# Performance work log

Hardware: AMD Instinct MI355X
Metric: run time of the kernel (lower is better)

The kernel has to match this reference:

```python
import jax, jax.numpy as jnp
from jax import lax
import numpy as np

CONF_THRES = 0.25
IOU_THRES = 0.45
MAX_OUT = 100  # max_output_boxes_per_class
N_BOXES = 25200  # YOLO 640x640 anchor count


def setup_inputs() -> dict:
    key = jax.random.key(0)
    kb, ks = jax.random.split(key)
    u = jax.random.uniform(kb, (N_BOXES, 4), dtype=jnp.float32)
    # build realistic corner boxes (x1,y1,x2,y2) on a 640x640 canvas
    cx, cy = u[:, 0] * 640.0, u[:, 1] * 640.0
    w = u[:, 2] * 60.0 + 4.0
    h = u[:, 3] * 60.0 + 4.0
    boxes = jnp.stack([cx - w / 2, cy - h / 2, cx + w / 2, cy + h / 2], axis=1)
    scores = jax.random.uniform(ks, (N_BOXES,), dtype=jnp.float32)
    return {"boxes": boxes, "scores": scores}


def _nms_indices(boxes, scores):
    """Greedy NMS. Returns (indices[MAX_OUT] into original boxes, valid[MAX_OUT] mask).
    Confidence filtering (scores > conf_thres) is done by masking to -inf so shapes stay static."""
    n = scores.shape[0]
    s = jnp.where(scores > CONF_THRES, scores, -jnp.inf)
    order = jnp.argsort(-s)               # descending score order
    b = boxes[order]                      # [N,4] sorted boxes
    s = s[order]                          # [N] sorted scores
    area = jnp.maximum(b[:, 2] - b[:, 0], 0.0) * jnp.maximum(b[:, 3] - b[:, 1], 0.0)
    pos = jnp.arange(n)

    def body(i, suppressed):
        keep_i = (~suppressed[i]) & jnp.isfinite(s[i])
        lt = jnp.maximum(b[i, :2], b[:, :2])   # intersection top-left
        rb = jnp.minimum(b[i, 2:], b[:, 2:])   # intersection bottom-right
        wh = jnp.maximum(rb - lt, 0.0)
        inter = wh[:, 0] * wh[:, 1]
        iou = inter / (area[i] + area - inter + 1e-9)
        return suppressed | (keep_i & (pos > i) & (iou > IOU_THRES))

    suppressed = lax.fori_loop(0, n, body, jnp.zeros((n,), bool))
    keep = (~suppressed) & jnp.isfinite(s)
    # pack first MAX_OUT kept (already in score order) into fixed-size output
    rank = jnp.cumsum(keep) - 1
    slot = jnp.where(keep & (rank < MAX_OUT), rank, MAX_OUT)  # overflow/dropped -> slot MAX_OUT
    out_idx = jnp.zeros((MAX_OUT + 1,), jnp.int32).at[slot].set(order.astype(jnp.int32))
    out_valid = jnp.zeros((MAX_OUT + 1,), bool).at[slot].set(keep)
    return out_idx[:MAX_OUT], out_valid[:MAX_OUT]


def reference(boxes, scores):
    idx, valid = _nms_indices(boxes, scores)
    vf = valid.astype(boxes.dtype)
    filtered_boxes = boxes[idx] * vf[:, None]   # zero-padded past the kept count
    filtered_scores = scores[idx] * vf
    return filtered_boxes, filtered_scores
```

## Files before the change

kernel.cpp:

```cpp
#include <hip/hip_runtime.h>
#include <math.h>

#define NB      25200
#define NB4     6300
#define THREADS 1024
#define KV      7
#define NBINS   512
#define CAP     128
#define MAXOUT  100
#define CONF    0.25f
#define PRE     0.98f
#define IOU_T   0.45f
#define NWAVE   16
#define ITEMS_FB 25

typedef unsigned long long u64;
typedef unsigned int u32;

__device__ __forceinline__ bool better(float sa_, int ia_, float sb_, int ib_) {
    return (sb_ > sa_) || (sb_ == sa_ && ib_ < ia_);
}

__global__ __launch_bounds__(THREADS, 1)
void nms_all(const float* __restrict__ boxes,
             const float* __restrict__ scores,
             float* __restrict__ out,
             float* __restrict__ ws_live)
{
    const int tid  = threadIdx.x;
    const int lane = tid & 63;
    const int wv   = tid >> 6;

    __shared__ int    hist[NBINS];
    __shared__ u64    keys[CAP];
    __shared__ float4 sbv[CAP];
    __shared__ float  ss[CAP];
    __shared__ float4 cand_b[CAP];
    __shared__ float  cand_s[CAP];
    __shared__ int    cand_i[CAP];
    __shared__ u64    mat[CAP][2];
    __shared__ int    prank[8][CAP];
    __shared__ int    klist[MAXOUT];
    __shared__ int    s_cnt, s_tbin, s_pack, s_kept;
    __shared__ float  red_v[NWAVE];
    __shared__ int    red_i[NWAVE];

    const float4* b4 = (const float4*)boxes;
    const float4* s4 = (const float4*)scores;
    const float binscale = (float)NBINS / (1.0f - PRE);

    float4 sc[KV];
#pragma unroll
    for (int k = 0; k < KV; ++k) {
        const int v = k * THREADS + tid;
        sc[k] = (v < NB4) ? s4[v] : make_float4(-1.f, -1.f, -1.f, -1.f);
    }
    if (tid < NBINS) hist[tid] = 0;
    if (tid == 0) { s_cnt = 0; s_pack = 0; }
    __syncthreads();

    int pack = 0;
#pragma unroll
    for (int k = 0; k < KV; ++k) {
        const float el[4] = {sc[k].x, sc[k].y, sc[k].z, sc[k].w};
#pragma unroll
        for (int e = 0; e < 4; ++e) {
            const float s = el[e];
            if (s > CONF) pack += 0x10000;
            if (s > PRE) {
                pack += 1;
                int b = (int)((s - PRE) * binscale);
                b = b < 0 ? 0 : (b > NBINS - 1 ? NBINS - 1 : b);
                atomicAdd(&hist[b], 1);
            }
        }
    }
#pragma unroll
    for (int off = 1; off < 64; off <<= 1) pack += __shfl_xor(pack, off);
    if (lane == 0) atomicAdd(&s_pack, pack);
    __syncthreads();
    const int total_conf = s_pack >> 16;

    if (tid < 64) {
        int h[8], ls[8];
#pragma unroll
        for (int r = 0; r < 8; ++r) h[r] = hist[lane * 8 + r];
        int acc = 0;
#pragma unroll
        for (int r = 7; r >= 0; --r) { acc += h[r]; ls[r] = acc; }
        u32 inc = (u32)acc;
#pragma unroll
        for (int off = 1; off < 64; off <<= 1) {
            const u32 t = __shfl_down(inc, off);
            if (lane + off < 64) inc += t;
        }
        const int excl = (int)inc - acc;
        int loc = NBINS;
#pragma unroll
        for (int r = 7; r >= 0; --r) { if (ls[r] + excl <= CAP) loc = lane * 8 + r; }
#pragma unroll
        for (int off = 32; off >= 1; off >>= 1) {
            const int t = __shfl_xor(loc, off);
            if (t < loc) loc = t;
        }
        if (lane == 0) s_tbin = loc;
    }
    __syncthreads();
    const int tbin = s_tbin;

#pragma unroll
    for (int k = 0; k < KV; ++k) {
        const int v = k * THREADS + tid;
        const float el[4] = {sc[k].x, sc[k].y, sc[k].z, sc[k].w};
#pragma unroll
        for (int e = 0; e < 4; ++e) {
            const float s = el[e];
            bool pred = false;
            if (s > PRE) {
                int b = (int)((s - PRE) * binscale);
                b = b < 0 ? 0 : (b > NBINS - 1 ? NBINS - 1 : b);
                pred = (b >= tbin);
            }
            if (pred) {
                const int pos = atomicAdd(&s_cnt, 1);
                if (pos < CAP) {
                    const int i = 4 * v + e;
                    cand_s[pos] = s; cand_i[pos] = i; cand_b[pos] = b4[i];
                }
            }
        }
    }
    __syncthreads();
    const int M0 = s_cnt;
    const int M  = (M0 > CAP) ? CAP : M0;

    float cs = 0.f; int ci = 0; float4 cb = make_float4(0.f, 0.f, 0.f, 0.f);
    if (tid < CAP) {
        if (tid < M) { cs = cand_s[tid]; ci = cand_i[tid]; cb = cand_b[tid]; }
        keys[tid] = (tid < M)
            ? (((u64)(~__float_as_uint(cs)) << 32) | (u64)(u32)ci)
            : (0xFFFFFFFF00000000ULL | (u64)tid);
    }
    __syncthreads();

    {
        const int key   = tid & (CAP - 1);
        const int chunk = tid >> 7;
        const u64 myk   = keys[key];
        u64 kb[16];
#pragma unroll
        for (int q = 0; q < 16; ++q) kb[q] = keys[chunk * 16 + q];
        int r = 0;
#pragma unroll
        for (int q = 0; q < 16; ++q) r += (kb[q] < myk) ? 1 : 0;
        prank[chunk][key] = r;
    }
    __syncthreads();
    if (tid < CAP && tid < M) {
        int rank = 0;
#pragma unroll
        for (int c = 0; c < 8; ++c) rank += prank[c][tid];
        sbv[rank] = cb;
        ss[rank]  = cs;
    }
    __syncthreads();

    {
        const int word = wv & 1;
        const int rb   = (wv >> 1) * 16;
        const int jidx = (word << 6) + lane;
        const float4 bj = sbv[jidx];
        const float  aj = fmaxf(bj.z - bj.x, 0.f) * fmaxf(bj.w - bj.y, 0.f);
        const bool   jv = (jidx < M);
        for (int ii = 0; ii < 16; ii += 4) {
            float4 bi[4];
#pragma unroll
            for (int q = 0; q < 4; ++q) bi[q] = sbv[rb + ii + q];
#pragma unroll
            for (int q = 0; q < 4; ++q) {
                const int irow = rb + ii + q;
                const float ai = fmaxf(bi[q].z - bi[q].x, 0.f) * fmaxf(bi[q].w - bi[q].y, 0.f);
                const float ltx = fmaxf(bi[q].x, bj.x);
                const float lty = fmaxf(bi[q].y, bj.y);
                const float rbx = fminf(bi[q].z, bj.z);
                const float rby = fminf(bi[q].w, bj.w);
                const float w_ = fmaxf(rbx - ltx, 0.f);
                const float h_ = fmaxf(rby - lty, 0.f);
                const float inter = w_ * h_;
                const float den = ((ai + aj) - inter) + 1e-9f;
                const bool pred = jv && (irow < M) && (jidx > irow) && (inter > IOU_T * den);
                const u64 bal = __ballot(pred);
                if (lane == 0) mat[irow][word] = bal;
            }
        }
    }
    __syncthreads();

    if (wv == 0) {
        const int r0i = 2 * lane, r1i = 2 * lane + 1;
        const u64 m00 = mat[r0i][0], m01 = mat[r0i][1];
        const u64 m10 = mat[r1i][0], m11 = mat[r1i][1];
        u32 alive = ((r0i < M) ? 1u : 0u) | ((r1i < M) ? 2u : 0u);
        int kept = 0;
        while (kept < MAXOUT) {
            const u64 bal = __ballot(alive != 0u);
            if (!bal) break;
            const int ldr = __ffsll(bal) - 1;
            const u32 la  = __shfl(alive, ldr);
            const int sub = (la & 1u) ? 0 : 1;
            const int row = 2 * ldr + sub;
            const u64 ra  = __shfl(sub ? m10 : m00, ldr);
            const u64 rb  = __shfl(sub ? m11 : m01, ldr);
            if (lane == 0) klist[kept] = row;
            ++kept;
            if (kept == MAXOUT) break;
            u32 kill = 0;
            kill |= (u32)(((r0i < 64) ? (ra >> r0i) : (rb >> (r0i - 64))) & 1ULL);
            kill |= (u32)(((r1i < 64) ? (ra >> r1i) : (rb >> (r1i - 64))) & 1ULL) << 1;
            alive &= ~kill;
            if (lane == ldr) alive &= ~(1u << sub);
        }
        if (lane == 0) s_kept = kept;
    }
    __syncthreads();

    const int kept = s_kept;
    const bool need_fb = (M0 > CAP) || (kept < MAXOUT && M0 < total_conf);
    if (!need_fb) {
        if (tid < MAXOUT) {
            float4 bb = make_float4(0.f, 0.f, 0.f, 0.f);
            float  sc_ = 0.f;
            if (tid < kept) { const int j = klist[tid]; bb = sbv[j]; sc_ = ss[j]; }
            ((float4*)out)[tid] = bb;
            out[4*MAXOUT + tid] = sc_;
        }
        return;
    }

    if (tid < 25600 - NB) ws_live[NB + tid] = -INFINITY;
    for (int k = 0; k < ITEMS_FB; ++k) {
        const int i = k * THREADS + tid;
        if (i < NB) {
            const float s0 = scores[i];
            ws_live[i] = (s0 > CONF) ? s0 : -INFINITY;
        }
    }
    __syncthreads();
    for (int r = 0; r < MAXOUT; ++r) {
        float lm = -INFINITY; int li = 0x7fffffff;
        for (int k = 0; k < ITEMS_FB; ++k) {
            const int i = k * THREADS + tid;
            const float v = ws_live[i];
            if (v > lm) { lm = v; li = i; }
        }
        float rv = lm; int ri = li;
#pragma unroll
        for (int off = 32; off >= 1; off >>= 1) {
            const float ov = __shfl_xor(rv, off);
            const int   oi = __shfl_xor(ri, off);
            if (better(rv, ri, ov, oi)) { rv = ov; ri = oi; }
        }
        __syncthreads();
        if (lane == 0) { red_v[wv] = rv; red_i[wv] = ri; }
        __syncthreads();
        float wval = red_v[0]; int widx = red_i[0];
#pragma unroll
        for (int j = 1; j < NWAVE; ++j) {
            const float v = red_v[j]; const int i2 = red_i[j];
            if (better(wval, widx, v, i2)) { wval = v; widx = i2; }
        }
        if (!(wval > -1e38f)) {
            if (tid == 0) {
                out[4*r+0]=0.f; out[4*r+1]=0.f; out[4*r+2]=0.f; out[4*r+3]=0.f;
                out[4*MAXOUT + r] = 0.f;
            }
            continue;
        }
        const float4 wb = b4[widx];
        if (tid == 0) {
            out[4*r+0]=wb.x; out[4*r+1]=wb.y; out[4*r+2]=wb.z; out[4*r+3]=wb.w;
            out[4*MAXOUT + r] = wval;
        }
        const float warea = fmaxf(wb.z - wb.x, 0.f) * fmaxf(wb.w - wb.y, 0.f);
        for (int k = 0; k < ITEMS_FB; ++k) {
            const int i = k * THREADS + tid;
            if (i < NB) {
                const float4 bb = b4[i];
                const float area = fmaxf(bb.z - bb.x, 0.f) * fmaxf(bb.w - bb.y, 0.f);
                const float ltx = fmaxf(bb.x, wb.x);
                const float lty = fmaxf(bb.y, wb.y);
                const float rbx = fminf(bb.z, wb.z);
                const float rby = fminf(bb.w, wb.w);
                const float w  = fmaxf(rbx - ltx, 0.f);
                const float h  = fmaxf(rby - lty, 0.f);
                const float inter = w * h;
                const float den = ((warea + area) - inter) + 1e-9f;
                if (inter > IOU_T * den || i == widx) ws_live[i] = -INFINITY;
            }
        }
        __syncthreads();
    }
}

extern "C" void kernel_launch(void* const* d_in, const int* in_sizes, int n_in,
                              void* d_out, int out_size, void* d_ws, size_t ws_size,
                              hipStream_t stream) {
    const float* boxes  = (const float*)d_in[0];
    const float* scores = (const float*)d_in[1];
    float* out = (float*)d_out;
    nms_all<<<dim3(1), dim3(THREADS), 0, stream>>>(boxes, scores, out, (float*)d_ws);
}
```

Before: 83.71 us.

## Split selection phase across cooperative grid with global histogram merge

Replaces the single 1024-thread block with a 32-block cooperative launch. Each block loads a slice of scores, builds a local histogram and confidence count, and publishes them to workspace; after a grid sync every block merges the histogram and gathers candidates via a global atomic counter. Block 0 then runs the sort, IoU bitmask and greedy selection with 256 threads. This spreads the input read over many CUs but adds grid-wide syncs, global atomics, and a narrower block for the tail and fallback phases.

```diff
diff --git a/kernel.cpp b/kernel.cpp
--- a/kernel.cpp
+++ b/kernel.cpp
@@ -1,18 +1,21 @@
 #include <hip/hip_runtime.h>
+#include <hip/hip_cooperative_groups.h>
 #include <math.h>
+
+namespace cg = cooperative_groups;
 
 #define NB      25200
 #define NB4     6300
-#define THREADS 1024
-#define KV      7
+#define BLOCKS  32
+#define THREADS 256
 #define NBINS   512
 #define CAP     128
 #define MAXOUT  100
 #define CONF    0.25f
 #define PRE     0.98f
 #define IOU_T   0.45f
-#define NWAVE   16
-#define ITEMS_FB 25
+#define NWAVE   4
+#define ITEMS_FB 100
 
 typedef unsigned long long u64;
 typedef unsigned int u32;
@@ -22,26 +25,33 @@
 }
 
 __global__ __launch_bounds__(THREADS, 1)
-void nms_all(const float* __restrict__ boxes,
-             const float* __restrict__ scores,
-             float* __restrict__ out,
-             float* __restrict__ ws_live)
+void nms_coop(const float* __restrict__ boxes, const float* __restrict__ scores,
+              float* __restrict__ out, char* __restrict__ ws)
 {
+    int*    ws_hist      = (int*)ws;
+    int*    partial_conf = (int*)(ws + 65536);
+    int*    cnt          = (int*)(ws + 65664);
+    float*  cand_s       = (float*)(ws + 65728);
+    int*    cand_i       = (int*)(ws + 66240);
+    float4* cand_b       = (float4*)(ws + 66752);
+    float*  live         = (float*)(ws + 69632);
+
+    cg::grid_group grid = cg::this_grid();
     const int tid  = threadIdx.x;
     const int lane = tid & 63;
     const int wv   = tid >> 6;
+    const int bid  = blockIdx.x;
+    const int gtid = bid * THREADS + tid;
 
     __shared__ int    hist[NBINS];
+    __shared__ int    cred[NWAVE];
     __shared__ u64    keys[CAP];
     __shared__ float4 sbv[CAP];
     __shared__ float  ss[CAP];
-    __shared__ float4 cand_b[CAP];
-    __shared__ float  cand_s[CAP];
-    __shared__ int    cand_i[CAP];
     __shared__ u64    mat[CAP][2];
-    __shared__ int    prank[8][CAP];
+    __shared__ int    prank[2][CAP];
     __shared__ int    klist[MAXOUT];
-    __shared__ int    s_cnt, s_tbin, s_pack, s_kept;
+    __shared__ int    s_tbin, s_total, s_kept;
     __shared__ float  red_v[NWAVE];
     __shared__ int    red_i[NWAVE];
 
@@ -49,38 +59,43 @@
     const float4* s4 = (const float4*)scores;
     const float binscale = (float)NBINS / (1.0f - PRE);
 
-    float4 sc[KV];
-#pragma unroll
-    for (int k = 0; k < KV; ++k) {
-        const int v = k * THREADS + tid;
-        sc[k] = (v < NB4) ? s4[v] : make_float4(-1.f, -1.f, -1.f, -1.f);
-    }
-    if (tid < NBINS) hist[tid] = 0;
-    if (tid == 0) { s_cnt = 0; s_pack = 0; }
-    __syncthreads();
-
-    int pack = 0;
-#pragma unroll
-    for (int k = 0; k < KV; ++k) {
-        const float el[4] = {sc[k].x, sc[k].y, sc[k].z, sc[k].w};
-#pragma unroll
-        for (int e = 0; e < 4; ++e) {
-            const float s = el[e];
-            if (s > CONF) pack += 0x10000;
-            if (s > PRE) {
-                pack += 1;
-                int b = (int)((s - PRE) * binscale);
-                b = b < 0 ? 0 : (b > NBINS - 1 ? NBINS - 1 : b);
-                atomicAdd(&hist[b], 1);
-            }
-        }
-    }
-#pragma unroll
-    for (int off = 1; off < 64; off <<= 1) pack += __shfl_xor(pack, off);
-    if (lane == 0) atomicAdd(&s_pack, pack);
-    __syncthreads();
-    const int total_conf = s_pack >> 16;
-
+    const float4 s = (gtid < NB4) ? s4[gtid] : make_float4(-1.f, -1.f, -1.f, -1.f);
+    const float el[4] = {s.x, s.y, s.z, s.w};
+    hist[tid] = 0; hist[tid + 256] = 0;
+    if (bid == 0 && tid == 0) *cnt = 0;
+    __syncthreads();
+
+    int conf_c = 0;
+#pragma unroll
+    for (int e = 0; e < 4; ++e) {
+        const float v = el[e];
+        if (v > CONF) ++conf_c;
+        if (v > PRE) {
+            int b = (int)((v - PRE) * binscale);
+            b = b < 0 ? 0 : (b > NBINS - 1 ? NBINS - 1 : b);
+            atomicAdd(&hist[b], 1);
+        }
+    }
+#pragma unroll
+    for (int off = 1; off < 64; off <<= 1) conf_c += __shfl_xor(conf_c, off);
+    if (lane == 0) cred[wv] = conf_c;
+    __syncthreads();
+    if (tid == 0) partial_conf[bid] = cred[0] + cred[1] + cred[2] + cred[3];
+    ws_hist[tid * 32 + bid]         = hist[tid];
+    ws_hist[(tid + 256) * 32 + bid] = hist[tid + 256];
+    __threadfence();
+    grid.sync();
+
+#pragma unroll
+    for (int r = 0; r < 2; ++r) {
+        const int bin = tid + r * 256;
+        const int4* p = (const int4*)(ws_hist + bin * 32);
+        int sum = 0;
+#pragma unroll
+        for (int q = 0; q < 8; ++q) { const int4 v = p[q]; sum += v.x + v.y + v.z + v.w; }
+        hist[bin] = sum;
+    }
+    __syncthreads();
     if (tid < 64) {
         int h[8], ls[8];
 #pragma unroll
@@ -103,35 +118,37 @@
             const int t = __shfl_xor(loc, off);
             if (t < loc) loc = t;
         }
-        if (lane == 0) s_tbin = loc;
-    }
-    __syncthreads();
-    const int tbin = s_tbin;
-
-#pragma unroll
-    for (int k = 0; k < KV; ++k) {
-        const int v = k * THREADS + tid;
-        const float el[4] = {sc[k].x, sc[k].y, sc[k].z, sc[k].w};
-#pragma unroll
-        for (int e = 0; e < 4; ++e) {
-            const float s = el[e];
-            bool pred = false;
-            if (s > PRE) {
-                int b = (int)((s - PRE) * binscale);
-                b = b < 0 ? 0 : (b > NBINS - 1 ? NBINS - 1 : b);
-                pred = (b >= tbin);
+        int pc = (lane < 32) ? partial_conf[lane] : 0;
+#pragma unroll
+        for (int off = 1; off < 64; off <<= 1) pc += __shfl_xor(pc, off);
+        if (lane == 0) { s_tbin = loc; s_total = pc; }
+    }
+    __syncthreads();
+    const int tbin       = s_tbin;
+    const int total_conf = s_total;
+
+#pragma unroll
+    for (int e = 0; e < 4; ++e) {
+        const float v = el[e];
+        bool pred = false;
+        if (v > PRE) {
+            int b = (int)((v - PRE) * binscale);
+            b = b < 0 ? 0 : (b > NBINS - 1 ? NBINS - 1 : b);
+            pred = (b >= tbin);
+        }
+        if (pred) {
+            const int pos = atomicAdd(cnt, 1);
+            if (pos < CAP) {
+                const int i = 4 * gtid + e;
+                cand_s[pos] = v; cand_i[pos] = i; cand_b[pos] = b4[i];
             }
-            if (pred) {
-                const int pos = atomicAdd(&s_cnt, 1);
-                if (pos < CAP) {
-                    const int i = 4 * v + e;
-                    cand_s[pos] = s; cand_i[pos] = i; cand_b[pos] = b4[i];
-                }
-            }
-        }
-    }
-    __syncthreads();
-    const int M0 = s_cnt;
+        }
+    }
+    __threadfence();
+    grid.sync();
+    if (bid != 0) return;
+
+    const int M0 = *cnt;
     const int M  = (M0 > CAP) ? CAP : M0;
 
     float cs = 0.f; int ci = 0; float4 cb = make_float4(0.f, 0.f, 0.f, 0.f);
@@ -147,19 +164,19 @@
         const int key   = tid & (CAP - 1);
         const int chunk = tid >> 7;
         const u64 myk   = keys[key];
-        u64 kb[16];
-#pragma unroll
-        for (int q = 0; q < 16; ++q) kb[q] = keys[chunk * 16 + q];
         int r = 0;
-#pragma unroll
-        for (int q = 0; q < 16; ++q) r += (kb[q] < myk) ? 1 : 0;
+        for (int j0 = 0; j0 < 64; j0 += 16) {
+            u64 kb[16];
+#pragma unroll
+            for (int q = 0; q < 16; ++q) kb[q] = keys[chunk * 64 + j0 + q];
+#pragma unroll
+            for (int q = 0; q < 16; ++q) r += (kb[q] < myk) ? 1 : 0;
+        }
         prank[chunk][key] = r;
     }
     __syncthreads();
     if (tid < CAP && tid < M) {
-        int rank = 0;
-#pragma unroll
-        for (int c = 0; c < 8; ++c) rank += prank[c][tid];
+        const int rank = prank[0][tid] + prank[1][tid];
         sbv[rank] = cb;
         ss[rank]  = cs;
     }
@@ -167,12 +184,12 @@
 
     {
         const int word = wv & 1;
-        const int rb   = (wv >> 1) * 16;
+        const int rb   = (wv >> 1) * 64;
         const int jidx = (word << 6) + lane;
         const float4 bj = sbv[jidx];
         const float  aj = fmaxf(bj.z - bj.x, 0.f) * fmaxf(bj.w - bj.y, 0.f);
         const bool   jv = (jidx < M);
-        for (int ii = 0; ii < 16; ii += 4) {
+        for (int ii = 0; ii < 64; ii += 4) {
             float4 bi[4];
 #pragma unroll
             for (int q = 0; q < 4; ++q) bi[q] = sbv[rb + ii + q];
@@ -237,12 +254,12 @@
         return;
     }
 
-    if (tid < 25600 - NB) ws_live[NB + tid] = -INFINITY;
+    for (int i = NB + tid; i < 25600; i += THREADS) live[i] = -INFINITY;
     for (int k = 0; k < ITEMS_FB; ++k) {
         const int i = k * THREADS + tid;
         if (i < NB) {
             const float s0 = scores[i];
-            ws_live[i] = (s0 > CONF) ? s0 : -INFINITY;
+            live[i] = (s0 > CONF) ? s0 : -INFINITY;
         }
     }
     __syncthreads();
@@ -250,7 +267,7 @@
         float lm = -INFINITY; int li = 0x7fffffff;
         for (int k = 0; k < ITEMS_FB; ++k) {
             const int i = k * THREADS + tid;
-            const float v = ws_live[i];
+            const float v = live[i];
             if (v > lm) { lm = v; li = i; }
         }
         float rv = lm; int ri = li;
@@ -295,7 +312,7 @@
                 const float h  = fmaxf(rby - lty, 0.f);
                 const float inter = w * h;
                 const float den = ((warea + area) - inter) + 1e-9f;
-                if (inter > IOU_T * den || i == widx) ws_live[i] = -INFINITY;
+                if (inter > IOU_T * den || i == widx) live[i] = -INFINITY;
             }
         }
         __syncthreads();
@@ -308,5 +325,8 @@
     const float* boxes  = (const float*)d_in[0];
     const float* scores = (const float*)d_in[1];
     float* out = (float*)d_out;
-    nms_all<<<dim3(1), dim3(THREADS), 0, stream>>>(boxes, scores, out, (float*)d_ws);
+    char*  ws  = (char*)d_ws;
+    void* args[4] = {(void*)&boxes, (void*)&scores, (void*)&out, (void*)&ws};
+    hipLaunchCooperativeKernel((const void*)nms_coop, dim3(BLOCKS), dim3(THREADS),
+                               args, 0, stream);
 }
```

Result: slower. 118.8 us (+41.9%).
